# Kernel optimization log

Hardware: AMD Instinct MI355X
Metric: run time of the kernel (lower is better)

The kernel has to match this reference:

```python
import math
import jax, jax.numpy as jnp
import numpy as np

B, S, D = 2, 2048, 4096
H = 32
HD = D // H  # 128
CLIP_QKV = 8.0
ALIBI_BIAS_MAX = 8
LN_EPS = 1e-5


def _get_alibi_slopes(total_num_heads: int, alibi_bias_max: int) -> np.ndarray:
    next_pow2 = 2 ** math.ceil(math.log2(total_num_heads))
    m = np.arange(1, next_pow2 + 1, dtype=np.float32) * (alibi_bias_max / next_pow2)
    slopes = 1.0 / np.power(2.0, m)
    if next_pow2 != total_num_heads:
        slopes = np.concatenate([slopes[1::2], slopes[::2]])[:total_num_heads]
    return slopes


ALIBI_SLOPES = jnp.asarray(_get_alibi_slopes(H, ALIBI_BIAS_MAX))  # [H]


def _layernorm(x, w, b):
    mu = jnp.mean(x, axis=-1, keepdims=True)
    var = jnp.mean(jnp.square(x - mu), axis=-1, keepdims=True)
    return (x - mu) * jax.lax.rsqrt(var + LN_EPS) * w + b


def setup_inputs() -> dict:
    key = jax.random.key(0)
    ks = jax.random.split(key, 3)
    scale_in = 1.0 / math.sqrt(D)
    return {
        "hidden_states": jax.random.normal(ks[0], (B, S, D), jnp.float32),
        "Wqkv": jax.random.normal(ks[1], (D, 3 * D), jnp.float32) * scale_in,
        "Wout": jax.random.normal(ks[2], (D, D), jnp.float32) * scale_in,
        "q_ln_w": jnp.ones((D,), jnp.float32),
        "q_ln_b": jnp.zeros((D,), jnp.float32),
        "k_ln_w": jnp.ones((D,), jnp.float32),
        "k_ln_b": jnp.zeros((D,), jnp.float32),
    }


def reference(hidden_states, Wqkv, Wout, q_ln_w, q_ln_b, k_ln_w, k_ln_b):
    # QKV projection + clamp
    qkv = jnp.clip(hidden_states @ Wqkv, -CLIP_QKV, CLIP_QKV)  # [B,S,3D]
    q, k, v = jnp.split(qkv, [D, 2 * D], axis=-1)
    # QK LayerNorm over full d_model (as in MPT qk_ln)
    q = _layernorm(q, q_ln_w, q_ln_b)
    k = _layernorm(k, k_ln_w, k_ln_b)
    # split heads
    q = q.reshape(B, S, H, HD)
    k = k.reshape(B, S, H, HD)
    v = v.reshape(B, S, H, HD)
    scale = HD ** (-0.5)
    scores = jnp.einsum("bqhd,bkhd->bhqk", q, k) * scale  # [B,H,S,S]
    # ALiBi bias: -slope * (i - j), causal mask j <= i
    pos = jnp.arange(S)
    dist = pos[:, None] - pos[None, :]  # [S,S], i - j
    bias = -ALIBI_SLOPES[:, None, None] * dist.astype(jnp.float32)  # [H,S,S]
    causal = dist >= 0
    scores = jnp.where(causal[None, None], scores + bias[None], -jnp.inf)
    attn = jax.nn.softmax(scores, axis=-1)
    out = jnp.einsum("bhqk,bkhd->bqhd", attn, v).reshape(B, S, D)
    return out @ Wout
```

## Files before the change

kernel.cpp:

```cpp
#include <hip/hip_runtime.h>
#include <hip/hip_bf16.h>
#include <stdint.h>

#define BB 2
#define SS 2048
#define DD 4096
#define HH 32
#define HDD 128

typedef unsigned short u16;
typedef unsigned int u32;

constexpr float CLIPV  = 8.0f;
constexpr float LN_EPS_ = 1e-5f;
constexpr float SCALE_ = 0.08838834764831845f;
constexpr float LOG2E_ = 1.4426950408889634f;

using f32x4 = __attribute__((ext_vector_type(4))) float;
using s16x8 = __attribute__((ext_vector_type(8))) short;

__device__ inline u16 f2bf(float f) {
  union { float f; u32 u; } v; v.f = f;
  u32 r = (v.u + 0x7FFFu + ((v.u >> 16) & 1u)) >> 16;
  return (u16)r;
}
__device__ inline float bf2f(u16 u) {
  union { u32 u; float f; } v; v.u = ((u32)u) << 16;
  return v.f;
}

typedef __attribute__((address_space(1))) void gvoid;
typedef __attribute__((address_space(3))) void lvoid;
__device__ inline void gload_lds16(const void* g, void* l) {
  __builtin_amdgcn_global_load_lds((gvoid*)g, (lvoid*)l, 16, 0, 0);
}

__device__ inline f32x4 mfma16(s16x8 a, s16x8 b, f32x4 c) {
  return __builtin_amdgcn_mfma_f32_16x16x32_bf16(a, b, c, 0, 0, 0);
}

__global__ void k_cvt_bf16(const float* __restrict__ in, u16* __restrict__ out, int nvec) {
  int i = blockIdx.x * 256 + threadIdx.x;
  if (i >= nvec) return;
  float4 a = ((const float4*)in)[i * 2];
  float4 b = ((const float4*)in)[i * 2 + 1];
  u16 tmp[8];
  tmp[0] = f2bf(a.x); tmp[1] = f2bf(a.y); tmp[2] = f2bf(a.z); tmp[3] = f2bf(a.w);
  tmp[4] = f2bf(b.x); tmp[5] = f2bf(b.y); tmp[6] = f2bf(b.z); tmp[7] = f2bf(b.w);
  ((uint4*)out)[i] = *(const uint4*)tmp;
}

__global__ void k_transpose_cvt(const float* __restrict__ src, u16* __restrict__ dst, int R, int C) {
  __shared__ float tile[32][33];
  int c0 = blockIdx.x * 32, r0 = blockIdx.y * 32;
  int tx = threadIdx.x & 31, ty = threadIdx.x >> 5;
  #pragma unroll
  for (int i = 0; i < 32; i += 8)
    tile[ty + i][tx] = src[(size_t)(r0 + ty + i) * C + (c0 + tx)];
  __syncthreads();
  #pragma unroll
  for (int i = 0; i < 32; i += 8)
    dst[(size_t)(c0 + ty + i) * R + (r0 + tx)] = f2bf(tile[tx][ty + i]);
}

__device__ __forceinline__ void stage_half(u16* ldsHalf, const u16* g, int K, int tid) {
  #pragma unroll
  for (int it = 0; it < 2; ++it) {
    int p = (it << 9) + tid;
    int row = p >> 3;
    int slotk = (p & 7) ^ (row & 7);
    gload_lds16(g + (size_t)row * K + (slotk << 3), ldsHalf + ((size_t)p << 3));
  }
}

#define DSR(dst, adr, IMM) \
  asm volatile("ds_read_b128 %0, %1 offset:" #IMM : "=v"(dst) : "v"(adr) : "memory")

#define RD_B1(a0, a1)            \
  DSR(bB_[0][0], a0, 4096);      \
  DSR(bB_[0][1], a1, 4096);      \
  DSR(bB_[1][0], a0, 6144);      \
  DSR(bB_[1][1], a1, 6144);

#define RD_A1(a0, a1)            \
  DSR(aN[0][0], a0, 8192);       \
  DSR(aN[0][1], a1, 8192);       \
  DSR(aN[1][0], a0, 10240);      \
  DSR(aN[1][1], a1, 10240);      \
  DSR(aN[2][0], a0, 12288);      \
  DSR(aN[2][1], a1, 12288);      \
  DSR(aN[3][0], a0, 14336);      \
  DSR(aN[3][1], a1, 14336);

#define RD_A0(a0, a1)            \
  DSR(aC[0][0], a0, 0);          \
  DSR(aC[0][1], a1, 0);          \
  DSR(aC[1][0], a0, 2048);       \
  DSR(aC[1][1], a1, 2048);       \
  DSR(aC[2][0], a0, 4096);       \
  DSR(aC[2][1], a1, 4096);       \
  DSR(aC[3][0], a0, 6144);       \
  DSR(aC[3][1], a1, 6144);

#define RD_B0(a0, a1)            \
  DSR(bA_[0][0], a0, 0);         \
  DSR(bA_[0][1], a1, 0);         \
  DSR(bA_[1][0], a0, 2048);      \
  DSR(bA_[1][1], a1, 2048);

#define LGKM(N)                                                    \
  asm volatile("s_waitcnt lgkmcnt(" #N ")" ::: "memory");          \
  __builtin_amdgcn_sched_barrier(0);

#define MQ(AF, BF, MB, JB)                                                    \
  _Pragma("unroll")                                                           \
  for (int i_ = 0; i_ < 4; ++i_) {                                            \
    _Pragma("unroll")                                                         \
    for (int jj_ = 0; jj_ < 2; ++jj_) {                                       \
      acc[(MB) + i_][(JB) + jj_] =                                            \
          mfma16(AF[i_][0], BF[jj_][0], acc[(MB) + i_][(JB) + jj_]);          \
      acc[(MB) + i_][(JB) + jj_] =                                            \
          mfma16(AF[i_][1], BF[jj_][1], acc[(MB) + i_][(JB) + jj_]);          \
    }                                                                         \
  }

template <int EPI>
__launch_bounds__(512)
__global__ void k_gemm256(const u16* __restrict__ A, const u16* __restrict__ Bt,
                          void* __restrict__ Cout, int M, int N, int K, int nBY) {
  __shared__ u16 lds[65536];
  u16* sA = lds;
  u16* sB = lds + 32768;
  const int tid = threadIdx.x;
  const int lane = tid & 63, w = tid >> 6;
  const int wm = w >> 2, wn = w & 3;
  const int lg = lane >> 4, lc = lane & 15;

  const int nwg = gridDim.x;
  const int cpx = nwg >> 3;
  const int id2 = (blockIdx.x & 7) * cpx + (blockIdx.x >> 3);
  const int bx = id2 / nBY, by = id2 % nBY;
  const int m0 = by * 256, n0 = bx * 256;

  const int NT = K >> 6;
  const u16* gA = A  + (size_t)m0 * K;
  const u16* gB = Bt + (size_t)n0 * K;

  const int xt0 = ((lg) ^ (lc & 7)) * 8;
  const int rowoff = lc * 64;

  const u32 aBase0 = (u32)(2 * (wm * 8192 + rowoff + xt0));
  const u32 bBase0 = (u32)(2 * (32768 + (wn >> 1) * 8192 + (wn & 1) * 4096 + rowoff + xt0));

  f32x4 acc[8][4];
  #pragma unroll
  for (int i = 0; i < 8; ++i)
    #pragma unroll
    for (int j = 0; j < 4; ++j) acc[i][j] = (f32x4){0.f, 0.f, 0.f, 0.f};

  stage_half(sA,         gA,                        K, tid);
  stage_half(sA + 8192,  gA + (size_t)128 * K,      K, tid);
  stage_half(sB,         gB,                        K, tid);
  stage_half(sB + 8192,  gB + (size_t)128 * K,      K, tid);
  stage_half(sB + 16384, gB + 64,                   K, tid);
  stage_half(sB + 24576, gB + (size_t)128 * K + 64, K, tid);
  stage_half(sA + 24576, gA + (size_t)128 * K + 64, K, tid);
  asm volatile("s_waitcnt vmcnt(0)" ::: "memory");
  __builtin_amdgcn_s_barrier();

  s16x8 aC[4][2], aN[4][2], bA_[2][2], bB_[2][2];
  {
    u32 a0 = aBase0, a1 = aBase0 ^ 64;
    u32 b0 = bBase0, b1 = bBase0 ^ 64;
    RD_A0(a0, a1)
    RD_B0(b0, b1)
  }

  for (int t = 0; t < NT; ++t) {
    const int d = t & 1;
    const bool m1 = (t + 1 < NT);
    const bool m2 = (t + 2 < NT);
    const u32 dx = d ? 32768u : 0u;
    const u32 a0 = aBase0 ^ dx, a1 = a0 ^ 64;
    const u32 b0 = bBase0 ^ dx, b1 = b0 ^ 64;
    const u32 an0 = a0 ^ 32768u, an1 = a1 ^ 32768u;
    const u32 bn0 = b0 ^ 32768u, bn1 = b1 ^ 32768u;

    RD_B1(b0, b1)
    if (m1) stage_half(sA + (d ^ 1) * 16384, gA + (size_t)(t + 1) * 64, K, tid);
    LGKM(4)
    __builtin_amdgcn_s_setprio(1);
    MQ(aC, bA_, 0, 0)
    __builtin_amdgcn_s_setprio(0);
    __builtin_amdgcn_s_barrier();

    RD_A1(a0, a1)
    if (m2) stage_half(sB + d * 16384, gB + (size_t)(t + 2) * 64, K, tid);
    LGKM(8)
    __builtin_amdgcn_s_setprio(1);
    MQ(aC, bB_, 0, 2)
    __builtin_amdgcn_s_setprio(0);
    __builtin_amdgcn_s_barrier();

    if (m2) stage_half(sB + d * 16384 + 8192, gB + (size_t)128 * K + (size_t)(t + 2) * 64, K, tid);
    LGKM(0)
    __builtin_amdgcn_s_setprio(1);
    MQ(aN, bA_, 4, 0)
    __builtin_amdgcn_s_setprio(0);
    if (m2) { asm volatile("s_waitcnt vmcnt(4)" ::: "memory"); }
    else    { asm volatile("s_waitcnt vmcnt(0)" ::: "memory"); }
    __builtin_amdgcn_s_barrier();

    if (m1) {
      RD_A0(an0, an1)
      RD_B0(bn0, bn1)
      if (m2) stage_half(sA + d * 16384 + 8192, gA + (size_t)128 * K + (size_t)(t + 2) * 64, K, tid);
    }
    __builtin_amdgcn_sched_barrier(0);
    __builtin_amdgcn_s_setprio(1);
    MQ(aN, bB_, 4, 2)
    __builtin_amdgcn_s_setprio(0);
    if (m2) { asm volatile("s_waitcnt vmcnt(2)" ::: "memory"); }
    else    { asm volatile("s_waitcnt vmcnt(0)" ::: "memory"); }
    __builtin_amdgcn_s_barrier();
  }

  #pragma unroll
  for (int i = 0; i < 8; ++i)
    #pragma unroll
    for (int j = 0; j < 4; ++j)
      #pragma unroll
      for (int r = 0; r < 4; ++r) {
        int m = m0 + wm * 128 + i * 16 + lg * 4 + r;
        int n = n0 + wn * 64 + j * 16 + lc;
        float v = acc[i][j][r];
        if (EPI == 0) {
          v = fminf(fmaxf(v, -CLIPV), CLIPV);
          ((u16*)Cout)[(size_t)m * N + n] = f2bf(v);
        } else {
          ((float*)Cout)[(size_t)m * N + n] = v;
        }
      }
}

__device__ inline void unpack8(uint4 u, float* f) {
  const u16* p = (const u16*)&u;
  #pragma unroll
  for (int j = 0; j < 8; ++j) f[j] = bf2f(p[j]);
}

__global__ void k_ln_reorder(const u16* __restrict__ qkv,
                             const float* __restrict__ qw, const float* __restrict__ qb,
                             const float* __restrict__ kw, const float* __restrict__ kb,
                             u16* __restrict__ Qo, u16* __restrict__ Ko) {
  const int row = blockIdx.x;
  const int b = row >> 11, s = row & 2047;
  const int t = threadIdx.x;
  const int lane = t & 63, w = t >> 6;
  const uint4* base = (const uint4*)(qkv + (size_t)row * (3 * DD));

  __shared__ float redsum[8], redss[8];

  uint4 q4[2], k4[2];
  q4[0] = base[t];        q4[1] = base[256 + t];
  k4[0] = base[512 + t];  k4[1] = base[768 + t];

  float qx[16], kx[16];
  unpack8(q4[0], qx); unpack8(q4[1], qx + 8);
  unpack8(k4[0], kx); unpack8(k4[1], kx + 8);

  float qs = 0.f, qss = 0.f, ks = 0.f, kss = 0.f;
  #pragma unroll
  for (int i = 0; i < 16; ++i) {
    qs += qx[i]; qss += qx[i] * qx[i];
    ks += kx[i]; kss += kx[i] * kx[i];
  }
  #pragma unroll
  for (int off = 1; off < 64; off <<= 1) {
    qs  += __shfl_xor(qs, off);  qss += __shfl_xor(qss, off);
    ks  += __shfl_xor(ks, off);  kss += __shfl_xor(kss, off);
  }
  if (lane == 0) { redsum[w] = qs; redss[w] = qss; redsum[4 + w] = ks; redss[4 + w] = kss; }
  __syncthreads();
  float qsum = redsum[0] + redsum[1] + redsum[2] + redsum[3];
  float qs2  = redss[0]  + redss[1]  + redss[2]  + redss[3];
  float ksum = redsum[4] + redsum[5] + redsum[6] + redsum[7];
  float ks2  = redss[4]  + redss[5]  + redss[6]  + redss[7];
  const float inv = 1.0f / (float)DD;
  float qmu = qsum * inv, qvar = qs2 * inv - qmu * qmu;
  float kmu = ksum * inv, kvar = ks2 * inv - kmu * kmu;
  float qrs = rsqrtf(qvar + LN_EPS_);
  float krs = rsqrtf(kvar + LN_EPS_);

  #pragma unroll
  for (int ch = 0; ch < 2; ++ch) {
    int c0 = ch * 2048 + t * 8;
    int hh = c0 >> 7, hd0 = c0 & 127;
    size_t idx = (((size_t)b * HH + hh) * SS + s) * HDD + hd0;
    {
      float4 w0 = *(const float4*)(qw + c0), w1 = *(const float4*)(qw + c0 + 4);
      float4 b0 = *(const float4*)(qb + c0), b1 = *(const float4*)(qb + c0 + 4);
      float wa[8] = {w0.x, w0.y, w0.z, w0.w, w1.x, w1.y, w1.z, w1.w};
      float ba[8] = {b0.x, b0.y, b0.z, b0.w, b1.x, b1.y, b1.z, b1.w};
      u16 tmp[8];
      #pragma unroll
      for (int j = 0; j < 8; ++j)
        tmp[j] = f2bf((qx[ch * 8 + j] - qmu) * qrs * wa[j] + ba[j]);
      *(uint4*)(Qo + idx) = *(const uint4*)tmp;
    }
    {
      float4 w0 = *(const float4*)(kw + c0), w1 = *(const float4*)(kw + c0 + 4);
      float4 b0 = *(const float4*)(kb + c0), b1 = *(const float4*)(kb + c0 + 4);
      float wa[8] = {w0.x, w0.y, w0.z, w0.w, w1.x, w1.y, w1.z, w1.w};
      float ba[8] = {b0.x, b0.y, b0.z, b0.w, b1.x, b1.y, b1.z, b1.w};
      u16 tmp[8];
      #pragma unroll
      for (int j = 0; j < 8; ++j)
        tmp[j] = f2bf((kx[ch * 8 + j] - kmu) * krs * wa[j] + ba[j]);
      *(uint4*)(Ko + idx) = *(const uint4*)tmp;
    }
  }
}

__global__ void k_transpose_v(const u16* __restrict__ qkv, u16* __restrict__ Vt) {
  __shared__ u16 ls[64 * 65];
  const int s0 = blockIdx.x * 64;
  const int hd0 = blockIdx.y * 64;
  const int bh = blockIdx.z;
  const int b = bh >> 5, h = bh & 31;
  const int t = threadIdx.x;
  const u16* src = qkv + (size_t)(b * SS + s0) * (3 * DD) + 2 * DD + h * HDD + hd0;
  #pragma unroll
  for (int it = 0; it < 4; ++it) {
    int idx = it * 256 + t;
    int sr = idx >> 4, hc = idx & 15;
    uint2 v = *(const uint2*)(src + (size_t)sr * (3 * DD) + hc * 4);
    const u16* pv = (const u16*)&v;
    #pragma unroll
    for (int j = 0; j < 4; ++j) ls[sr * 65 + hc * 4 + j] = pv[j];
  }
  __syncthreads();
  u16* dst = Vt + ((size_t)bh * HDD + hd0) * SS + s0;
  #pragma unroll
  for (int it = 0; it < 4; ++it) {
    int idx = it * 256 + t;
    int hd = idx >> 4, sc = idx & 15;
    u16 tmp[4];
    #pragma unroll
    for (int j = 0; j < 4; ++j) tmp[j] = ls[(4 * sc + j) * 65 + hd];
    *(uint2*)(dst + (size_t)hd * SS + 4 * sc) = *(const uint2*)tmp;
  }
}

__global__ __launch_bounds__(512)
void k_attn(const u16* __restrict__ Qg, const u16* __restrict__ Kg,
            const u16* __restrict__ Vt, u16* __restrict__ Og) {
  const int bid = blockIdx.x;
  const int id2 = ((bid & 7) << 7) + (bid >> 3);
  const int bh = id2 >> 4;
  const int qt = id2 & 15;
  const int b = bh >> 5, h = bh & 31;
  const int t = threadIdx.x;
  const int lane = t & 63, w = t >> 6;
  const int lg = lane >> 4, lc = lane & 15;
  const float slope = exp2f(-0.25f * (float)(h + 1));

  __shared__ u16 lK[2][8192];
  __shared__ u16 lV[2][8192];
  __shared__ u16 lP[8][1024];

  const int q0 = qt * 128 + w * 16;
  const size_t bhS = (size_t)bh * SS;
  const u16* Kbase = Kg + bhS * HDD;
  const u16* Vbase = Vt + bhS * HDD;

  s16x8 qf[4];
  {
    const u16* qrow = Qg + (bhS + q0 + lc) * HDD;
    #pragma unroll
    for (int kt = 0; kt < 4; ++kt) qf[kt] = *(const s16x8*)(qrow + kt * 32 + lg * 8);
  }

  f32x4 ot[8];
  #pragma unroll
  for (int hf = 0; hf < 8; ++hf) ot[hf] = (f32x4){0.f, 0.f, 0.f, 0.f};
  float m_r = -1e30f, l_r = 0.f;

  #define STAGE_KV(D, KV0)                                                         \
    {                                                                              \
      _Pragma("unroll")                                                            \
      for (int it_ = 0; it_ < 2; ++it_) {                                          \
        int sl = it_ * 512 + t;                                                    \
        int row = sl >> 4, k16 = sl & 15;                                          \
        gload_lds16(Kbase + (size_t)((KV0) + row) * HDD + ((k16 ^ (row & 7)) * 8), \
                    &lK[D][sl * 8]);                                               \
      }                                                                            \
      _Pragma("unroll")                                                            \
      for (int it_ = 0; it_ < 2; ++it_) {                                          \
        int sl = it_ * 512 + t;                                                    \
        int row = sl >> 3, k8 = sl & 7;                                            \
        gload_lds16(Vbase + (size_t)row * SS + (KV0) + ((k8 ^ (row & 7)) * 8),     \
                    &lV[D][sl * 8]);                                               \
      }                                                                            \
    }

  STAGE_KV(0, 0)
  __syncthreads();

  const int nt = 2 * qt + 2;
  for (int itn = 0; itn < nt; ++itn) {
    const int d = itn & 1;
    const int kv0 = itn * 64;
    if (itn + 1 < nt) STAGE_KV(d ^ 1, kv0 + 64)

    if (kv0 <= q0 + 15) {
      f32x4 st[4];
      #pragma unroll
      for (int i = 0; i < 4; ++i) {
        st[i] = (f32x4){0.f, 0.f, 0.f, 0.f};
        #pragma unroll
        for (int kt = 0; kt < 4; ++kt) {
          int r = i * 16 + lc;
          const s16x8 ka = *(const s16x8*)&lK[d][r * 128 + (((kt * 4 + lg) ^ (r & 7)) * 8)];
          st[i] = mfma16(ka, qf[kt], st[i]);
        }
      }

      float sc[4][4];
      float pm = -1e30f;
      const int qg = q0 + lc;
      #pragma unroll
      for (int i = 0; i < 4; ++i)
        #pragma unroll
        for (int r = 0; r < 4; ++r) {
          int kv = kv0 + i * 16 + lg * 4 + r;
          float x = (kv <= qg) ? st[i][r] * SCALE_ - slope * (float)(qg - kv) : -1e30f;
          sc[i][r] = x;
          pm = fmaxf(pm, x);
        }
      pm = fmaxf(pm, __shfl_xor(pm, 16));
      pm = fmaxf(pm, __shfl_xor(pm, 32));
      float m_new = fmaxf(m_r, pm);
      float alpha = exp2f((m_r - m_new) * LOG2E_);
      float rsum = 0.f;
      #pragma unroll
      for (int i = 0; i < 4; ++i) {
        float p0 = exp2f((sc[i][0] - m_new) * LOG2E_);
        float p1 = exp2f((sc[i][1] - m_new) * LOG2E_);
        float p2 = exp2f((sc[i][2] - m_new) * LOG2E_);
        float p3 = exp2f((sc[i][3] - m_new) * LOG2E_);
        rsum += (p0 + p1) + (p2 + p3);
        u32 dlo, dhi;
        asm("v_cvt_pk_bf16_f32 %0, %1, %2" : "=v"(dlo) : "v"(p0), "v"(p1));
        asm("v_cvt_pk_bf16_f32 %0, %1, %2" : "=v"(dhi) : "v"(p2), "v"(p3));
        int addr = lc * 64 + (((4 * i + lg) ^ (2 * (lc & 7))) * 4);
        uint2 val; val.x = dlo; val.y = dhi;
        *(uint2*)&lP[w][addr] = val;
      }
      rsum += __shfl_xor(rsum, 16);
      rsum += __shfl_xor(rsum, 32);
      l_r = l_r * alpha + rsum;
      m_r = m_new;

      #pragma unroll
      for (int hf = 0; hf < 8; ++hf) {
        ot[hf][0] *= alpha; ot[hf][1] *= alpha; ot[hf][2] *= alpha; ot[hf][3] *= alpha;
      }

      #pragma unroll
      for (int ks = 0; ks < 2; ++ks) {
        const int m = 4 * ks + lg;
        const s16x8 pa = *(const s16x8*)&lP[w][lc * 64 + ((m ^ (lc & 7)) * 8)];
        #pragma unroll
        for (int hf = 0; hf < 8; ++hf) {
          int row = hf * 16 + lc;
          const s16x8 vb = *(const s16x8*)&lV[d][row * 64 + ((m ^ (row & 7)) * 8)];
          ot[hf] = mfma16(vb, pa, ot[hf]);
        }
      }
    }
    __syncthreads();
  }
  #undef STAGE_KV

  float linv = 1.f / l_r;
  const size_t obase = ((size_t)(b * SS + q0 + lc)) * DD + h * HDD;
  #pragma unroll
  for (int hf = 0; hf < 8; ++hf) {
    u16 tmp[4];
    #pragma unroll
    for (int r = 0; r < 4; ++r) tmp[r] = f2bf(ot[hf][r] * linv);
    *(uint2*)&Og[obase + hf * 16 + lg * 4] = *(const uint2*)tmp;
  }
}

extern "C" void kernel_launch(void* const* d_in, const int* in_sizes, int n_in,
                              void* d_out, int out_size, void* d_ws, size_t ws_size,
                              hipStream_t stream) {
  const float* hidden = (const float*)d_in[0];
  const float* Wqkv   = (const float*)d_in[1];
  const float* Wout   = (const float*)d_in[2];
  const float* qw     = (const float*)d_in[3];
  const float* qb     = (const float*)d_in[4];
  const float* kw     = (const float*)d_in[5];
  const float* kb     = (const float*)d_in[6];
  float* out = (float*)d_out;
  char* ws = (char*)d_ws;

  u16* Xb    = (u16*)(ws);
  u16* WqkvT = (u16*)(ws + 33554432);
  u16* Qb    = (u16*)(ws + 33554432);
  u16* Kb    = (u16*)(ws + 67108864);
  u16* Vtb   = (u16*)(ws + 100663296);
  u16* WoutT = (u16*)(ws + 134217728);
  u16* qkv   = (u16*)(ws + 167772160);
  u16* attnO = Xb;

  k_cvt_bf16<<<8192, 256, 0, stream>>>(hidden, Xb, 2097152);
  k_transpose_cvt<<<dim3(12288 / 32, 4096 / 32), 256, 0, stream>>>(Wqkv, WqkvT, 4096, 12288);
  k_transpose_cvt<<<dim3(4096 / 32, 4096 / 32), 256, 0, stream>>>(Wout, WoutT, 4096, 4096);
  k_gemm256<0><<<768, 512, 0, stream>>>(Xb, WqkvT, qkv, 4096, 12288, 4096, 16);
  k_ln_reorder<<<4096, 256, 0, stream>>>(qkv, qw, qb, kw, kb, Qb, Kb);
  k_transpose_v<<<dim3(SS / 64, HDD / 64, BB * HH), 256, 0, stream>>>(qkv, Vtb);
  k_attn<<<1024, 512, 0, stream>>>(Qb, Kb, Vtb, attnO);
  k_gemm256<1><<<256, 512, 0, stream>>>(attnO, WoutT, out, 4096, 4096, 4096, 16);
}
```

Baseline: 798.0 us.

## Iterate KV tiles in reverse and skip redundant online-softmax rescaling

The attention loop now walks KV tiles from the diagonal backwards. With ALiBi, the highest scores tend to sit near the diagonal, so the running max settles early, and the output rescale is skipped whenever no lane's max grows, using a wave-wide __any check. Score computation also precomputes per-lane slope offsets and splits off a fast path without causal masking for fully unmasked tiles. The cost is a divergent branch per tile; the softmax result is unchanged up to rounding.

Measured after the change: 792.4 us. Within noise of the previous version (-0.7%).

```diff
diff --git a/kernel.cpp b/kernel.cpp
--- a/kernel.cpp
+++ b/kernel.cpp
@@ -381,10 +381,17 @@
     for (int kt = 0; kt < 4; ++kt) qf[kt] = *(const s16x8*)(qrow + kt * 32 + lg * 8);
   }
 
+  float sKt[16];
+  #pragma unroll
+  for (int i = 0; i < 4; ++i)
+    #pragma unroll
+    for (int r = 0; r < 4; ++r) sKt[i * 4 + r] = slope * (float)(i * 16 + lg * 4 + r);
+
   f32x4 ot[8];
   #pragma unroll
   for (int hf = 0; hf < 8; ++hf) ot[hf] = (f32x4){0.f, 0.f, 0.f, 0.f};
   float m_r = -1e30f, l_r = 0.f;
+  const int qg = q0 + lc;
 
   #define STAGE_KV(D, KV0)                                                         \
     {                                                                              \
@@ -404,14 +411,14 @@
       }                                                                            \
     }
 
-  STAGE_KV(0, 0)
+  const int nt = 2 * qt + 2;
+  STAGE_KV((nt - 1) & 1, (nt - 1) * 64)
   __syncthreads();
 
-  const int nt = 2 * qt + 2;
-  for (int itn = 0; itn < nt; ++itn) {
+  for (int itn = nt - 1; itn >= 0; --itn) {
     const int d = itn & 1;
     const int kv0 = itn * 64;
-    if (itn + 1 < nt) STAGE_KV(d ^ 1, kv0 + 64)
+    if (itn > 0) STAGE_KV(d ^ 1, kv0 - 64)
 
     if (kv0 <= q0 + 15) {
       f32x4 st[4];
@@ -428,27 +435,50 @@
 
       float sc[4][4];
       float pm = -1e30f;
-      const int qg = q0 + lc;
-      #pragma unroll
-      for (int i = 0; i < 4; ++i)
+      const float c0 = slope * (float)(kv0 - qg);
+      if (kv0 + 63 <= q0) {
         #pragma unroll
-        for (int r = 0; r < 4; ++r) {
-          int kv = kv0 + i * 16 + lg * 4 + r;
-          float x = (kv <= qg) ? st[i][r] * SCALE_ - slope * (float)(qg - kv) : -1e30f;
-          sc[i][r] = x;
-          pm = fmaxf(pm, x);
-        }
+        for (int i = 0; i < 4; ++i)
+          #pragma unroll
+          for (int r = 0; r < 4; ++r) {
+            float x = fmaf(st[i][r], SCALE_, c0 + sKt[i * 4 + r]);
+            sc[i][r] = x;
+            pm = fmaxf(pm, x);
+          }
+      } else {
+        const int thr2 = (qg - kv0) - lg * 4;
+        #pragma unroll
+        for (int i = 0; i < 4; ++i)
+          #pragma unroll
+          for (int r = 0; r < 4; ++r) {
+            float x = ((i * 16 + r) <= thr2)
+                          ? fmaf(st[i][r], SCALE_, c0 + sKt[i * 4 + r])
+                          : -1e30f;
+            sc[i][r] = x;
+            pm = fmaxf(pm, x);
+          }
+      }
       pm = fmaxf(pm, __shfl_xor(pm, 16));
       pm = fmaxf(pm, __shfl_xor(pm, 32));
-      float m_new = fmaxf(m_r, pm);
-      float alpha = exp2f((m_r - m_new) * LOG2E_);
+
+      if (__any(pm > m_r)) {
+        float m_new = fmaxf(m_r, pm);
+        float alpha = exp2f((m_r - m_new) * LOG2E_);
+        #pragma unroll
+        for (int hf = 0; hf < 8; ++hf) {
+          ot[hf][0] *= alpha; ot[hf][1] *= alpha; ot[hf][2] *= alpha; ot[hf][3] *= alpha;
+        }
+        l_r *= alpha;
+        m_r = m_new;
+      }
+
       float rsum = 0.f;
       #pragma unroll
       for (int i = 0; i < 4; ++i) {
-        float p0 = exp2f((sc[i][0] - m_new) * LOG2E_);
-        float p1 = exp2f((sc[i][1] - m_new) * LOG2E_);
-        float p2 = exp2f((sc[i][2] - m_new) * LOG2E_);
-        float p3 = exp2f((sc[i][3] - m_new) * LOG2E_);
+        float p0 = exp2f((sc[i][0] - m_r) * LOG2E_);
+        float p1 = exp2f((sc[i][1] - m_r) * LOG2E_);
+        float p2 = exp2f((sc[i][2] - m_r) * LOG2E_);
+        float p3 = exp2f((sc[i][3] - m_r) * LOG2E_);
         rsum += (p0 + p1) + (p2 + p3);
         u32 dlo, dhi;
         asm("v_cvt_pk_bf16_f32 %0, %1, %2" : "=v"(dlo) : "v"(p0), "v"(p1));
@@ -459,13 +489,7 @@
       }
       rsum += __shfl_xor(rsum, 16);
       rsum += __shfl_xor(rsum, 32);
-      l_r = l_r * alpha + rsum;
-      m_r = m_new;
-
-      #pragma unroll
-      for (int hf = 0; hf < 8; ++hf) {
-        ot[hf][0] *= alpha; ot[hf][1] *= alpha; ot[hf][2] *= alpha; ot[hf][3] *= alpha;
-      }
+      l_r += rsum;
 
       #pragma unroll
       for (int ks = 0; ks < 2; ++ks) {
```
